# Performance work log

Measured on AMD Instinct MI355X. Metric: run time of the kernel, lower is better.

Reference implementation:

```python
import jax, jax.numpy as jnp
import numpy as np

B, N, M, D = 16, 128, 64, 512
H = 4
K = D // H  # head_dim = 128
L = 3      # num_labels


def setup_inputs() -> dict:
    key = jax.random.key(0)
    ks = jax.random.split(key, 16)
    s = 0.02
    return {
        "word": jax.random.normal(ks[0], (B, N, D), jnp.float32),
        "rel": jax.random.normal(ks[1], (B, M, D), jnp.float32),
        "mask": jnp.ones((B, M), jnp.float32),
        "Wn_w": jax.random.normal(ks[2], (D, D), jnp.float32) * s,
        "Wn_b": jnp.zeros((D,), jnp.float32),
        "Wr_w": jax.random.normal(ks[3], (D, D), jnp.float32) * s,
        "Wr_b": jnp.zeros((D,), jnp.float32),
        "lin_w": jax.random.normal(ks[4], (H, D, K), jnp.float32) * s,
        "lin_b": jnp.zeros((H, K), jnp.float32),
        "score_w": jax.random.normal(ks[5], (H, K), jnp.float32) * s,
        "score_b": jnp.zeros((H,), jnp.float32),
        "final_w": jax.random.normal(ks[6], (D, D), jnp.float32) * s,
        "final_b": jnp.zeros((D,), jnp.float32),
        "fc_w": jax.random.normal(ks[7], (D, L), jnp.float32) * s,
        "fc_b": jnp.zeros((L,), jnp.float32),
    }


def reference(word, rel, mask, Wn_w, Wn_b, Wr_w, Wr_b, lin_w, lin_b,
              score_w, score_b, final_w, final_b, fc_w, fc_b):
    # projections (dropout = identity in eval mode)
    w = word @ Wn_w + Wn_b                     # [B,N,D]
    r = rel @ Wr_w + Wr_b                      # [B,M,D]
    # outer-product hadamard + relu            # [B,N,M,D]
    had = jax.nn.relu(w[:, :, None, :] * r[:, None, :, :])
    # per-head linear projection, vectorized over heads
    t = jnp.einsum('bnmd,hdk->bnmhk', had, lin_w) + lin_b  # [B,N,M,H,K]
    # per-head scalar score + softmax over M (the dim=-1 of [B,N,M])
    s = jnp.einsum('bnmhk,hk->bnmh', t, score_w) + score_b  # [B,N,M,H]
    wts = jax.nn.softmax(s, axis=2) * mask[:, None, :, None]
    # masked weighted sum over M, then mean over N
    head = jnp.einsum('bnmh,bnmhk->bnhk', wts, t)           # [B,N,H,K]
    head = head.mean(axis=1).reshape(head.shape[0], H * K)  # [B,D] (concat heads)
    out = head @ final_w + final_b
    out = jax.nn.relu(out)
    logits = out @ fc_w + fc_b                               # [B,L]
    return logits
```

## Files before the change

kernel.cpp:

```cpp
#include <hip/hip_runtime.h>
#include <math.h>


#define OFF_W   0
#define OFF_R   (2048*512)
#define OFF_V   (OFF_R + 1024*512)
#define OFF_S   (OFF_V + 2048)
#define OFF_G   (OFF_S + 64*8192)
#define OFF_SW  (OFF_G + 64*512)
#define OFF_HM  (OFF_SW + 256)

__global__ __launch_bounds__(256) void proj_gemm(
    const float* __restrict__ word, const float* __restrict__ rel,
    const float* __restrict__ Wn_w, const float* __restrict__ Wn_b,
    const float* __restrict__ Wr_w, const float* __restrict__ Wr_b,
    const float* __restrict__ lin_w, const float* __restrict__ score_w,
    float* __restrict__ ws)
{
    int blk = blockIdx.x;
    if (blk >= 384) {
        int gid = (blk - 384) * 256 + threadIdx.x;
        int h = gid >> 9, d = gid & 511;
        const float* lw = lin_w + (size_t)(h * 512 + d) * 128;
        const float* sw = score_w + h * 128;
        float acc = 0.f;
        #pragma unroll 4
        for (int k = 0; k < 128; k += 4) {
            float4 a = *(const float4*)(lw + k);
            float4 b = *(const float4*)(sw + k);
            acc = fmaf(a.x, b.x, acc); acc = fmaf(a.y, b.y, acc);
            acc = fmaf(a.z, b.z, acc); acc = fmaf(a.w, b.w, acc);
        }
        ws[OFF_V + h * 512 + d] = 0.5f * acc;
        return;
    }
    const float *A, *W, *bias;
    float* C;
    int rowTile, colTile;
    if (blk < 256) {
        A = word; W = Wn_w; bias = Wn_b; C = ws + OFF_W;
        rowTile = blk >> 3; colTile = blk & 7;
    } else {
        int b2 = blk - 256;
        A = rel; W = Wr_w; bias = Wr_b; C = ws + OFF_R;
        rowTile = b2 >> 3; colTile = b2 & 7;
    }
    const int row0 = rowTile * 64, col0 = colTile * 64;

    __shared__ float As[16][68];
    __shared__ float Bs[16][64];

    const int t  = threadIdx.x;
    const int tx = t & 15, ty = t >> 4;
    const int lr = t >> 2, lk = (t & 3) << 2;
    const int bk = t >> 4, bc = (t & 15) << 2;

    float acc[4][4] = {};

    for (int k0 = 0; k0 < 512; k0 += 16) {
        float4 a4 = *(const float4*)(A + (size_t)(row0 + lr) * 512 + k0 + lk);
        As[lk + 0][lr] = a4.x; As[lk + 1][lr] = a4.y;
        As[lk + 2][lr] = a4.z; As[lk + 3][lr] = a4.w;
        *(float4*)&Bs[bk][bc] = *(const float4*)(W + (size_t)(k0 + bk) * 512 + col0 + bc);
        __syncthreads();
        #pragma unroll
        for (int kk = 0; kk < 16; kk++) {
            float4 av = *(float4*)&As[kk][ty << 2];
            float4 bv = *(float4*)&Bs[kk][tx << 2];
            float aa[4] = {av.x, av.y, av.z, av.w};
            float bb[4] = {bv.x, bv.y, bv.z, bv.w};
            #pragma unroll
            for (int i = 0; i < 4; i++)
                #pragma unroll
                for (int j = 0; j < 4; j++)
                    acc[i][j] = fmaf(aa[i], bb[j], acc[i][j]);
        }
        __syncthreads();
    }
    float4 bv = *(const float4*)(bias + col0 + (tx << 2));
    float bb[4] = {bv.x, bv.y, bv.z, bv.w};
    #pragma unroll
    for (int i = 0; i < 4; i++) {
        float4 o;
        o.x = acc[i][0] + bb[0]; o.y = acc[i][1] + bb[1];
        o.z = acc[i][2] + bb[2]; o.w = acc[i][3] + bb[3];
        *(float4*)(C + (size_t)(row0 + (ty << 2) + i) * 512 + col0 + (tx << 2)) = o;
    }
}

__global__ __launch_bounds__(256) void scores_sm(
    const float* __restrict__ mask, float* __restrict__ ws)
{
    const int blk = blockIdx.x;
    const int nq = blk & 3, bh = blk >> 2, h = bh & 3, b = bh >> 2;
    const int n0 = nq * 32;

    const float* wbase = ws + OFF_W + (size_t)(b * 128) * 512;
    const float* rbase = ws + OFF_R + (size_t)(b * 64) * 512;
    float* wtsT = ws + OFF_S + (size_t)bh * 8192;

    __shared__ float v2s[512];
    __shared__ float maskl[64];
    __shared__ float As[16][68], Aa[16][68];
    __shared__ float Bs[16][36], Ba[16][36];
    __shared__ float sl[64][37];
    __shared__ float invl[33];

    const int t = threadIdx.x;
    if (t < 128) *(float4*)&v2s[t * 4] = *(const float4*)(ws + OFF_V + h * 512 + t * 4);
    if (t < 64) maskl[t] = mask[b * 64 + t];
    __syncthreads();

    const int ty = t >> 4, tx = t & 15;
    const int am = t >> 2, akq = (t & 3) * 4;
    const int bn = t >> 2, bkq = (t & 3) * 4;

    float acc[4][2] = {};

    for (int k0 = 0; k0 < 512; k0 += 16) {
        {
            float4 r4 = *(const float4*)(rbase + (size_t)am * 512 + k0 + akq);
            float4 vv = *(const float4*)&v2s[k0 + akq];
            As[akq + 0][am] = r4.x * vv.x; Aa[akq + 0][am] = fabsf(r4.x) * vv.x;
            As[akq + 1][am] = r4.y * vv.y; Aa[akq + 1][am] = fabsf(r4.y) * vv.y;
            As[akq + 2][am] = r4.z * vv.z; Aa[akq + 2][am] = fabsf(r4.z) * vv.z;
            As[akq + 3][am] = r4.w * vv.w; Aa[akq + 3][am] = fabsf(r4.w) * vv.w;
        }
        if (t < 128) {
            float4 w4 = *(const float4*)(wbase + (size_t)(n0 + bn) * 512 + k0 + bkq);
            Bs[bkq + 0][bn] = w4.x; Ba[bkq + 0][bn] = fabsf(w4.x);
            Bs[bkq + 1][bn] = w4.y; Ba[bkq + 1][bn] = fabsf(w4.y);
            Bs[bkq + 2][bn] = w4.z; Ba[bkq + 2][bn] = fabsf(w4.z);
            Bs[bkq + 3][bn] = w4.w; Ba[bkq + 3][bn] = fabsf(w4.w);
        }
        __syncthreads();
        #pragma unroll
        for (int kk = 0; kk < 16; kk++) {
            float4 a  = *(float4*)&As[kk][ty * 4];
            float4 aa = *(float4*)&Aa[kk][ty * 4];
            float2 bv  = *(float2*)&Bs[kk][tx * 2];
            float2 bav = *(float2*)&Ba[kk][tx * 2];
            float a_[4]  = {a.x, a.y, a.z, a.w};
            float aa_[4] = {aa.x, aa.y, aa.z, aa.w};
            #pragma unroll
            for (int i = 0; i < 4; i++) {
                acc[i][0] = fmaf(a_[i], bv.x,  acc[i][0]);
                acc[i][0] = fmaf(aa_[i], bav.x, acc[i][0]);
                acc[i][1] = fmaf(a_[i], bv.y,  acc[i][1]);
                acc[i][1] = fmaf(aa_[i], bav.y, acc[i][1]);
            }
        }
        __syncthreads();
    }
    #pragma unroll
    for (int i = 0; i < 4; i++) {
        sl[ty * 4 + i][tx * 2 + 0] = acc[i][0];
        sl[ty * 4 + i][tx * 2 + 1] = acc[i][1];
    }
    __syncthreads();

    if (t < 32) {
        const int n = t;
        float mx = sl[0][n];
        #pragma unroll
        for (int m = 1; m < 64; m++) mx = fmaxf(mx, sl[m][n]);
        float esum = 0.f, emsum = 0.f;
        #pragma unroll
        for (int m = 0; m < 64; m++) {
            float e = expf(sl[m][n] - mx);
            sl[m][n] = e;
            esum += e;
            emsum = fmaf(e, maskl[m], emsum);
        }
        float inv = 1.0f / esum;
        invl[n] = inv;
        float swq = emsum * inv;
        #pragma unroll
        for (int off = 16; off > 0; off >>= 1)
            swq += __shfl_xor(swq, off);
        if (t == 0) ws[OFF_SW + bh * 4 + nq] = swq;
    }
    __syncthreads();

    const int wn = t >> 3;
    const int wm = (t & 7) * 8;
    const float inv = invl[wn];
    float o[8];
    #pragma unroll
    for (int e2 = 0; e2 < 8; e2++)
        o[e2] = sl[wm + e2][wn] * inv * maskl[wm + e2];
    float4 o0; o0.x = o[0]; o0.y = o[1]; o0.z = o[2]; o0.w = o[3];
    float4 o1; o1.x = o[4]; o1.y = o[5]; o1.z = o[6]; o1.w = o[7];
    *(float4*)(wtsT + (size_t)(n0 + wn) * 64 + wm)     = o0;
    *(float4*)(wtsT + (size_t)(n0 + wn) * 64 + wm + 4) = o1;
}

__global__ __launch_bounds__(256) void gstep_kernel(float* __restrict__ ws)
{
    const int blk = blockIdx.x;
    const int dtile = blk & 7, bh = blk >> 3;
    const int b = bh >> 2;
    const int d0 = dtile * 64;
    const float* wtsT  = ws + OFF_S + (size_t)bh * 8192;
    const float* wbase = ws + OFF_W + (size_t)(b * 128) * 512;
    const float* rbase = ws + OFF_R + (size_t)(b * 64) * 512;

    __shared__ float As[16][68];
    __shared__ float Bs[16][68];
    __shared__ float Ba[16][68];
    __shared__ float red[16][68];

    const int t = threadIdx.x;
    const int tx = t & 15, ty = t >> 4;
    const int an_r = t >> 4, am4 = (t & 15) * 4;
    const int bn = t >> 4, bd4 = (t & 15) * 4;

    float accC[4][4] = {}, accA[4][4] = {};

    for (int n0 = 0; n0 < 128; n0 += 16) {
        *(float4*)&As[an_r][am4] =
            *(const float4*)(wtsT + (size_t)(n0 + an_r) * 64 + am4);
        float4 b4 = *(const float4*)(wbase + (size_t)(n0 + bn) * 512 + d0 + bd4);
        *(float4*)&Bs[bn][bd4] = b4;
        float4 bb; bb.x = fabsf(b4.x); bb.y = fabsf(b4.y);
        bb.z = fabsf(b4.z); bb.w = fabsf(b4.w);
        *(float4*)&Ba[bn][bd4] = bb;
        __syncthreads();
        #pragma unroll
        for (int kk = 0; kk < 16; kk++) {
            float4 av  = *(float4*)&As[kk][ty * 4];
            float4 bv  = *(float4*)&Bs[kk][tx * 4];
            float4 bav = *(float4*)&Ba[kk][tx * 4];
            float av_[4]  = {av.x, av.y, av.z, av.w};
            float bv_[4]  = {bv.x, bv.y, bv.z, bv.w};
            float bav_[4] = {bav.x, bav.y, bav.z, bav.w};
            #pragma unroll
            for (int i = 0; i < 4; i++)
                #pragma unroll
                for (int j = 0; j < 4; j++) {
                    accC[i][j] = fmaf(av_[i], bv_[j],  accC[i][j]);
                    accA[i][j] = fmaf(av_[i], bav_[j], accA[i][j]);
                }
        }
        __syncthreads();
    }
    float g0 = 0.f, g1 = 0.f, g2 = 0.f, g3 = 0.f;
    #pragma unroll
    for (int i = 0; i < 4; i++) {
        float4 rv = *(const float4*)(rbase + (size_t)(ty * 4 + i) * 512 + d0 + tx * 4);
        g0 = fmaf(rv.x, accC[i][0], g0); g0 = fmaf(fabsf(rv.x), accA[i][0], g0);
        g1 = fmaf(rv.y, accC[i][1], g1); g1 = fmaf(fabsf(rv.y), accA[i][1], g1);
        g2 = fmaf(rv.z, accC[i][2], g2); g2 = fmaf(fabsf(rv.z), accA[i][2], g2);
        g3 = fmaf(rv.w, accC[i][3], g3); g3 = fmaf(fabsf(rv.w), accA[i][3], g3);
    }
    float4 gg; gg.x = g0; gg.y = g1; gg.z = g2; gg.w = g3;
    *(float4*)&red[ty][tx * 4] = gg;
    __syncthreads();
    if (t < 64) {
        float s = 0.f;
        #pragma unroll
        for (int q = 0; q < 16; q++) s += red[q][t];
        ws[OFF_G + (size_t)bh * 512 + d0 + t] = 0.5f * s;
    }
}

__global__ __launch_bounds__(256) void headmean_kernel(
    const float* __restrict__ lin_w, const float* __restrict__ lin_b,
    float* __restrict__ ws)
{
    const int blk = blockIdx.x;
    const int kt = blk & 3, bh = blk >> 2, b = bh >> 2, h = bh & 3;
    const int t = threadIdx.x;
    const int dg = t >> 5, kk = t & 31;
    const int k = kt * 32 + kk;

    __shared__ float Gs[512];
    __shared__ float red[8][33];

    Gs[t]       = ws[OFF_G + (size_t)bh * 512 + t];
    Gs[t + 256] = ws[OFF_G + (size_t)bh * 512 + t + 256];
    __syncthreads();

    const float* lwp = lin_w + ((size_t)h * 512 + dg * 64) * 128 + k;
    const float* gp = Gs + dg * 64;
    float acc = 0.f;
    #pragma unroll 8
    for (int d = 0; d < 64; d++)
        acc = fmaf(gp[d], lwp[(size_t)d * 128], acc);
    red[dg][kk] = acc;
    __syncthreads();
    if (t < 32) {
        float s = 0.f;
        #pragma unroll
        for (int q = 0; q < 8; q++) s += red[q][t];
        const float SWv = ws[OFF_SW + bh * 4 + 0] + ws[OFF_SW + bh * 4 + 1]
                        + ws[OFF_SW + bh * 4 + 2] + ws[OFF_SW + bh * 4 + 3];
        s = fmaf(lin_b[h * 128 + kt * 32 + t], SWv, s);
        ws[OFF_HM + (size_t)b * 512 + h * 128 + kt * 32 + t] = s * (1.0f / 128.0f);
    }
}

__global__ __launch_bounds__(256) void final_logits(
    const float* __restrict__ final_w, const float* __restrict__ final_b,
    const float* __restrict__ fc_w, const float* __restrict__ fc_b,
    const float* __restrict__ ws, float* __restrict__ out)
{
    const int blk = blockIdx.x;
    const int jt = blk & 15, b = blk >> 4;
    const int t = threadIdx.x;
    const int dg = t >> 5, jj = t & 31;
    const int j = jt * 32 + jj;

    __shared__ float hs[512];
    __shared__ float red[8][33];
    __shared__ float osl[32];

    hs[t]       = ws[OFF_HM + (size_t)b * 512 + t];
    hs[t + 256] = ws[OFF_HM + (size_t)b * 512 + t + 256];
    __syncthreads();

    const float* fwp = final_w + (size_t)(dg * 64) * 512 + j;
    const float* hp = hs + dg * 64;
    float acc = 0.f;
    #pragma unroll 8
    for (int d = 0; d < 64; d++)
        acc = fmaf(hp[d], fwp[(size_t)d * 512], acc);
    red[dg][jj] = acc;
    __syncthreads();
    if (t < 32) {
        float s = 0.f;
        #pragma unroll
        for (int q = 0; q < 8; q++) s += red[q][t];
        osl[t] = fmaxf(s + final_b[jt * 32 + t], 0.f);
    }
    __syncthreads();
    if (t < 96) {
        const int l = t >> 5, j2 = t & 31;
        float val = osl[j2] * fc_w[(jt * 32 + j2) * 3 + l];
        #pragma unroll
        for (int off = 16; off > 0; off >>= 1)
            val += __shfl_xor(val, off);
        if (j2 == 0) atomicAdd(out + b * 3 + l, val);
    }
    if (jt == 0 && t < 3) atomicAdd(out + b * 3 + t, fc_b[t]);
}

extern "C" void kernel_launch(void* const* d_in, const int* in_sizes, int n_in,
                              void* d_out, int out_size, void* d_ws, size_t ws_size,
                              hipStream_t stream)
{
    const float* word    = (const float*)d_in[0];
    const float* rel     = (const float*)d_in[1];
    const float* mask    = (const float*)d_in[2];
    const float* Wn_w    = (const float*)d_in[3];
    const float* Wn_b    = (const float*)d_in[4];
    const float* Wr_w    = (const float*)d_in[5];
    const float* Wr_b    = (const float*)d_in[6];
    const float* lin_w   = (const float*)d_in[7];
    const float* lin_b   = (const float*)d_in[8];
    const float* score_w = (const float*)d_in[9];
    const float* final_w = (const float*)d_in[11];
    const float* final_b = (const float*)d_in[12];
    const float* fc_w    = (const float*)d_in[13];
    const float* fc_b    = (const float*)d_in[14];
    float* ws  = (float*)d_ws;
    float* out = (float*)d_out;

    hipMemsetAsync(out, 0, 16 * 3 * sizeof(float), stream);

    proj_gemm<<<392, 256, 0, stream>>>(word, rel, Wn_w, Wn_b, Wr_w, Wr_b,
                                       lin_w, score_w, ws);
    scores_sm<<<256, 256, 0, stream>>>(mask, ws);
    gstep_kernel<<<512, 256, 0, stream>>>(ws);
    headmean_kernel<<<256, 256, 0, stream>>>(lin_w, lin_b, ws);
    final_logits<<<256, 256, 0, stream>>>(final_w, final_b, fc_w, fc_b, ws, out);
}
```

Before: 191.2 us.

## Double-buffer score GEMM, parallelize softmax, fuse head-mean and final layers

The score kernel now double-buffers its shared-memory tiles and prefetches the next k-slice into registers, which removes one barrier per iteration. It also recomputes |w| on the fly instead of storing a second tile. The softmax reduction is spread across all 256 threads instead of 32. The head-mean and final/logits kernels are merged into a single 16-block kernel that writes outputs directly, removing the memset, the atomics and one launch. The trade-off is that the fused epilogue runs on only 16 blocks with long serial dot products, so it may underuse the GPU.

Measured after the change: 218.0 us. +14.0%, slower.

```diff
diff --git a/kernel.cpp b/kernel.cpp
--- a/kernel.cpp
+++ b/kernel.cpp
@@ -8,7 +8,6 @@
 #define OFF_S   (OFF_V + 2048)
 #define OFF_G   (OFF_S + 64*8192)
 #define OFF_SW  (OFF_G + 64*512)
-#define OFF_HM  (OFF_SW + 256)
 
 __global__ __launch_bounds__(256) void proj_gemm(
     const float* __restrict__ word, const float* __restrict__ rel,
@@ -101,98 +100,125 @@
 
     __shared__ float v2s[512];
     __shared__ float maskl[64];
-    __shared__ float As[16][68], Aa[16][68];
-    __shared__ float Bs[16][36], Ba[16][36];
-    __shared__ float sl[64][37];
-    __shared__ float invl[33];
+    __shared__ float Arv[2][16][68];
+    __shared__ float Ara[2][16][68];
+    __shared__ float Wl[2][16][36];
+    __shared__ float sl[64][33];
+    __shared__ float pmax[8][33], psum[8][33], pms[8][33];
 
     const int t = threadIdx.x;
     if (t < 128) *(float4*)&v2s[t * 4] = *(const float4*)(ws + OFF_V + h * 512 + t * 4);
     if (t < 64) maskl[t] = mask[b * 64 + t];
-    __syncthreads();
-
-    const int ty = t >> 4, tx = t & 15;
-    const int am = t >> 2, akq = (t & 3) * 4;
-    const int bn = t >> 2, bkq = (t & 3) * 4;
+
+    const int tm = t & 15, tn = t >> 4;
+    const int sm = t >> 2, sk = (t & 3) * 4;
+    const int wn = t >> 2, wk = (t & 3) * 4;
+    __syncthreads();
+
+    {
+        float4 r4 = *(const float4*)(rbase + (size_t)sm * 512 + sk);
+        float4 vv = *(const float4*)&v2s[sk];
+        Arv[0][sk + 0][sm] = r4.x * vv.x; Ara[0][sk + 0][sm] = fabsf(r4.x) * vv.x;
+        Arv[0][sk + 1][sm] = r4.y * vv.y; Ara[0][sk + 1][sm] = fabsf(r4.y) * vv.y;
+        Arv[0][sk + 2][sm] = r4.z * vv.z; Ara[0][sk + 2][sm] = fabsf(r4.z) * vv.z;
+        Arv[0][sk + 3][sm] = r4.w * vv.w; Ara[0][sk + 3][sm] = fabsf(r4.w) * vv.w;
+        if (t < 128) {
+            float4 w4 = *(const float4*)(wbase + (size_t)(n0 + wn) * 512 + wk);
+            Wl[0][wk + 0][wn] = w4.x; Wl[0][wk + 1][wn] = w4.y;
+            Wl[0][wk + 2][wn] = w4.z; Wl[0][wk + 3][wn] = w4.w;
+        }
+    }
+    __syncthreads();
 
     float acc[4][2] = {};
-
-    for (int k0 = 0; k0 < 512; k0 += 16) {
-        {
-            float4 r4 = *(const float4*)(rbase + (size_t)am * 512 + k0 + akq);
-            float4 vv = *(const float4*)&v2s[k0 + akq];
-            As[akq + 0][am] = r4.x * vv.x; Aa[akq + 0][am] = fabsf(r4.x) * vv.x;
-            As[akq + 1][am] = r4.y * vv.y; Aa[akq + 1][am] = fabsf(r4.y) * vv.y;
-            As[akq + 2][am] = r4.z * vv.z; Aa[akq + 2][am] = fabsf(r4.z) * vv.z;
-            As[akq + 3][am] = r4.w * vv.w; Aa[akq + 3][am] = fabsf(r4.w) * vv.w;
-        }
-        if (t < 128) {
-            float4 w4 = *(const float4*)(wbase + (size_t)(n0 + bn) * 512 + k0 + bkq);
-            Bs[bkq + 0][bn] = w4.x; Ba[bkq + 0][bn] = fabsf(w4.x);
-            Bs[bkq + 1][bn] = w4.y; Ba[bkq + 1][bn] = fabsf(w4.y);
-            Bs[bkq + 2][bn] = w4.z; Ba[bkq + 2][bn] = fabsf(w4.z);
-            Bs[bkq + 3][bn] = w4.w; Ba[bkq + 3][bn] = fabsf(w4.w);
-        }
-        __syncthreads();
+    int buf = 0;
+    for (int s = 0; s < 32; s++) {
+        float4 r4n, w4n;
+        const int k0n = (s + 1) * 16;
+        if (s < 31) {
+            r4n = *(const float4*)(rbase + (size_t)sm * 512 + k0n + sk);
+            if (t < 128)
+                w4n = *(const float4*)(wbase + (size_t)(n0 + wn) * 512 + k0n + wk);
+        }
         #pragma unroll
         for (int kk = 0; kk < 16; kk++) {
-            float4 a  = *(float4*)&As[kk][ty * 4];
-            float4 aa = *(float4*)&Aa[kk][ty * 4];
-            float2 bv  = *(float2*)&Bs[kk][tx * 2];
-            float2 bav = *(float2*)&Ba[kk][tx * 2];
-            float a_[4]  = {a.x, a.y, a.z, a.w};
-            float aa_[4] = {aa.x, aa.y, aa.z, aa.w};
-            #pragma unroll
-            for (int i = 0; i < 4; i++) {
-                acc[i][0] = fmaf(a_[i], bv.x,  acc[i][0]);
-                acc[i][0] = fmaf(aa_[i], bav.x, acc[i][0]);
-                acc[i][1] = fmaf(a_[i], bv.y,  acc[i][1]);
-                acc[i][1] = fmaf(aa_[i], bav.y, acc[i][1]);
+            float4 rv = *(float4*)&Arv[buf][kk][tm * 4];
+            float4 ra = *(float4*)&Ara[buf][kk][tm * 4];
+            float2 wv = *(float2*)&Wl[buf][kk][tn * 2];
+            float wax = fabsf(wv.x), way = fabsf(wv.y);
+            acc[0][0] = fmaf(rv.x, wv.x, acc[0][0]); acc[0][0] = fmaf(ra.x, wax, acc[0][0]);
+            acc[1][0] = fmaf(rv.y, wv.x, acc[1][0]); acc[1][0] = fmaf(ra.y, wax, acc[1][0]);
+            acc[2][0] = fmaf(rv.z, wv.x, acc[2][0]); acc[2][0] = fmaf(ra.z, wax, acc[2][0]);
+            acc[3][0] = fmaf(rv.w, wv.x, acc[3][0]); acc[3][0] = fmaf(ra.w, wax, acc[3][0]);
+            acc[0][1] = fmaf(rv.x, wv.y, acc[0][1]); acc[0][1] = fmaf(ra.x, way, acc[0][1]);
+            acc[1][1] = fmaf(rv.y, wv.y, acc[1][1]); acc[1][1] = fmaf(ra.y, way, acc[1][1]);
+            acc[2][1] = fmaf(rv.z, wv.y, acc[2][1]); acc[2][1] = fmaf(ra.z, way, acc[2][1]);
+            acc[3][1] = fmaf(rv.w, wv.y, acc[3][1]); acc[3][1] = fmaf(ra.w, way, acc[3][1]);
+        }
+        if (s < 31) {
+            float4 vv = *(const float4*)&v2s[k0n + sk];
+            const int nb = buf ^ 1;
+            Arv[nb][sk + 0][sm] = r4n.x * vv.x; Ara[nb][sk + 0][sm] = fabsf(r4n.x) * vv.x;
+            Arv[nb][sk + 1][sm] = r4n.y * vv.y; Ara[nb][sk + 1][sm] = fabsf(r4n.y) * vv.y;
+            Arv[nb][sk + 2][sm] = r4n.z * vv.z; Ara[nb][sk + 2][sm] = fabsf(r4n.z) * vv.z;
+            Arv[nb][sk + 3][sm] = r4n.w * vv.w; Ara[nb][sk + 3][sm] = fabsf(r4n.w) * vv.w;
+            if (t < 128) {
+                Wl[nb][wk + 0][wn] = w4n.x; Wl[nb][wk + 1][wn] = w4n.y;
+                Wl[nb][wk + 2][wn] = w4n.z; Wl[nb][wk + 3][wn] = w4n.w;
             }
         }
         __syncthreads();
-    }
+        buf ^= 1;
+    }
+
     #pragma unroll
     for (int i = 0; i < 4; i++) {
-        sl[ty * 4 + i][tx * 2 + 0] = acc[i][0];
-        sl[ty * 4 + i][tx * 2 + 1] = acc[i][1];
-    }
-    __syncthreads();
-
-    if (t < 32) {
-        const int n = t;
-        float mx = sl[0][n];
-        #pragma unroll
-        for (int m = 1; m < 64; m++) mx = fmaxf(mx, sl[m][n]);
-        float esum = 0.f, emsum = 0.f;
-        #pragma unroll
-        for (int m = 0; m < 64; m++) {
-            float e = expf(sl[m][n] - mx);
-            sl[m][n] = e;
-            esum += e;
-            emsum = fmaf(e, maskl[m], emsum);
-        }
-        float inv = 1.0f / esum;
-        invl[n] = inv;
-        float swq = emsum * inv;
-        #pragma unroll
-        for (int off = 16; off > 0; off >>= 1)
-            swq += __shfl_xor(swq, off);
-        if (t == 0) ws[OFF_SW + bh * 4 + nq] = swq;
-    }
-    __syncthreads();
-
-    const int wn = t >> 3;
-    const int wm = (t & 7) * 8;
-    const float inv = invl[wn];
+        sl[tm * 4 + i][tn * 2 + 0] = acc[i][0];
+        sl[tm * 4 + i][tn * 2 + 1] = acc[i][1];
+    }
+    __syncthreads();
+
+    const int col = t & 31, seg = t >> 5;
+    {
+        float mx = sl[seg * 8 + 0][col];
+        #pragma unroll
+        for (int q = 1; q < 8; q++) mx = fmaxf(mx, sl[seg * 8 + q][col]);
+        pmax[seg][col] = mx;
+    }
+    __syncthreads();
+    float gmx = pmax[0][col];
+    #pragma unroll
+    for (int q = 1; q < 8; q++) gmx = fmaxf(gmx, pmax[q][col]);
+    float es[8], ps = 0.f, pm = 0.f;
+    #pragma unroll
+    for (int q = 0; q < 8; q++) {
+        int m = seg * 8 + q;
+        float e = expf(sl[m][col] - gmx);
+        es[q] = e; ps += e; pm = fmaf(e, maskl[m], pm);
+    }
+    psum[seg][col] = ps; pms[seg][col] = pm;
+    __syncthreads();
+    float tot = psum[0][col];
+    #pragma unroll
+    for (int q = 1; q < 8; q++) tot += psum[q][col];
+    const float inv = 1.0f / tot;
     float o[8];
     #pragma unroll
-    for (int e2 = 0; e2 < 8; e2++)
-        o[e2] = sl[wm + e2][wn] * inv * maskl[wm + e2];
+    for (int q = 0; q < 8; q++) o[q] = es[q] * inv * maskl[seg * 8 + q];
     float4 o0; o0.x = o[0]; o0.y = o[1]; o0.z = o[2]; o0.w = o[3];
     float4 o1; o1.x = o[4]; o1.y = o[5]; o1.z = o[6]; o1.w = o[7];
-    *(float4*)(wtsT + (size_t)(n0 + wn) * 64 + wm)     = o0;
-    *(float4*)(wtsT + (size_t)(n0 + wn) * 64 + wm + 4) = o1;
+    *(float4*)(wtsT + (size_t)(n0 + col) * 64 + seg * 8)     = o0;
+    *(float4*)(wtsT + (size_t)(n0 + col) * 64 + seg * 8 + 4) = o1;
+    if (seg == 0) {
+        float pmt = pms[0][col];
+        #pragma unroll
+        for (int q = 1; q < 8; q++) pmt += pms[q][col];
+        float swc = pmt * inv;
+        #pragma unroll
+        for (int off = 16; off > 0; off >>= 1)
+            swc += __shfl_xor(swc, off);
+        if (col == 0) ws[OFF_SW + bh * 4 + nq] = swc;
+    }
 }
 
 __global__ __launch_bounds__(256) void gstep_kernel(float* __restrict__ ws)
@@ -264,85 +290,70 @@
     }
 }
 
-__global__ __launch_bounds__(256) void headmean_kernel(
+__global__ __launch_bounds__(256) void epilogue_kernel(
     const float* __restrict__ lin_w, const float* __restrict__ lin_b,
-    float* __restrict__ ws)
-{
-    const int blk = blockIdx.x;
-    const int kt = blk & 3, bh = blk >> 2, b = bh >> 2, h = bh & 3;
-    const int t = threadIdx.x;
-    const int dg = t >> 5, kk = t & 31;
-    const int k = kt * 32 + kk;
-
-    __shared__ float Gs[512];
-    __shared__ float red[8][33];
-
-    Gs[t]       = ws[OFF_G + (size_t)bh * 512 + t];
-    Gs[t + 256] = ws[OFF_G + (size_t)bh * 512 + t + 256];
-    __syncthreads();
-
-    const float* lwp = lin_w + ((size_t)h * 512 + dg * 64) * 128 + k;
-    const float* gp = Gs + dg * 64;
-    float acc = 0.f;
-    #pragma unroll 8
-    for (int d = 0; d < 64; d++)
-        acc = fmaf(gp[d], lwp[(size_t)d * 128], acc);
-    red[dg][kk] = acc;
-    __syncthreads();
-    if (t < 32) {
-        float s = 0.f;
-        #pragma unroll
-        for (int q = 0; q < 8; q++) s += red[q][t];
-        const float SWv = ws[OFF_SW + bh * 4 + 0] + ws[OFF_SW + bh * 4 + 1]
-                        + ws[OFF_SW + bh * 4 + 2] + ws[OFF_SW + bh * 4 + 3];
-        s = fmaf(lin_b[h * 128 + kt * 32 + t], SWv, s);
-        ws[OFF_HM + (size_t)b * 512 + h * 128 + kt * 32 + t] = s * (1.0f / 128.0f);
-    }
-}
-
-__global__ __launch_bounds__(256) void final_logits(
     const float* __restrict__ final_w, const float* __restrict__ final_b,
     const float* __restrict__ fc_w, const float* __restrict__ fc_b,
     const float* __restrict__ ws, float* __restrict__ out)
 {
-    const int blk = blockIdx.x;
-    const int jt = blk & 15, b = blk >> 4;
-    const int t = threadIdx.x;
-    const int dg = t >> 5, jj = t & 31;
-    const int j = jt * 32 + jj;
-
+    const int b = blockIdx.x, t = threadIdx.x;
+    __shared__ float Gs[2048];
     __shared__ float hs[512];
-    __shared__ float red[8][33];
-    __shared__ float osl[32];
-
-    hs[t]       = ws[OFF_HM + (size_t)b * 512 + t];
-    hs[t + 256] = ws[OFF_HM + (size_t)b * 512 + t + 256];
-    __syncthreads();
-
-    const float* fwp = final_w + (size_t)(dg * 64) * 512 + j;
-    const float* hp = hs + dg * 64;
-    float acc = 0.f;
-    #pragma unroll 8
-    for (int d = 0; d < 64; d++)
-        acc = fmaf(hp[d], fwp[(size_t)d * 512], acc);
-    red[dg][jj] = acc;
-    __syncthreads();
-    if (t < 32) {
-        float s = 0.f;
-        #pragma unroll
-        for (int q = 0; q < 8; q++) s += red[q][t];
-        osl[t] = fmaxf(s + final_b[jt * 32 + t], 0.f);
-    }
-    __syncthreads();
-    if (t < 96) {
-        const int l = t >> 5, j2 = t & 31;
-        float val = osl[j2] * fc_w[(jt * 32 + j2) * 3 + l];
-        #pragma unroll
-        for (int off = 16; off > 0; off >>= 1)
-            val += __shfl_xor(val, off);
-        if (j2 == 0) atomicAdd(out + b * 3 + l, val);
-    }
-    if (jt == 0 && t < 3) atomicAdd(out + b * 3 + t, fc_b[t]);
+    __shared__ float os[512];
+    __shared__ float SWs[4];
+
+    const float* G = ws + OFF_G + (size_t)b * 2048;
+    #pragma unroll
+    for (int i = 0; i < 8; i++) Gs[t + 256 * i] = G[t + 256 * i];
+    if (t < 4) {
+        const float* swq = ws + OFF_SW + (size_t)(b * 4 + t) * 4;
+        SWs[t] = (swq[0] + swq[1]) + (swq[2] + swq[3]);
+    }
+    __syncthreads();
+
+    #pragma unroll
+    for (int i = 0; i < 2; i++) {
+        int idx = t + 256 * i;
+        int h = idx >> 7, k = idx & 127;
+        const float* lwp = lin_w + ((size_t)h * 512) * 128 + k;
+        const float* gp = Gs + h * 512;
+        float a0 = 0.f, a1 = 0.f, a2 = 0.f, a3 = 0.f;
+        for (int d = 0; d < 512; d += 4) {
+            a0 = fmaf(gp[d + 0], lwp[(size_t)(d + 0) * 128], a0);
+            a1 = fmaf(gp[d + 1], lwp[(size_t)(d + 1) * 128], a1);
+            a2 = fmaf(gp[d + 2], lwp[(size_t)(d + 2) * 128], a2);
+            a3 = fmaf(gp[d + 3], lwp[(size_t)(d + 3) * 128], a3);
+        }
+        float acc = (a0 + a1) + (a2 + a3) + lin_b[h * 128 + k] * SWs[h];
+        hs[idx] = acc * (1.0f / 128.0f);
+    }
+    __syncthreads();
+
+    #pragma unroll
+    for (int i = 0; i < 2; i++) {
+        int j = t + 256 * i;
+        const float* fwp = final_w + j;
+        float a0 = 0.f, a1 = 0.f, a2 = 0.f, a3 = 0.f;
+        for (int d = 0; d < 512; d += 4) {
+            a0 = fmaf(hs[d + 0], fwp[(size_t)(d + 0) * 512], a0);
+            a1 = fmaf(hs[d + 1], fwp[(size_t)(d + 1) * 512], a1);
+            a2 = fmaf(hs[d + 2], fwp[(size_t)(d + 2) * 512], a2);
+            a3 = fmaf(hs[d + 3], fwp[(size_t)(d + 3) * 512], a3);
+        }
+        os[j] = fmaxf((a0 + a1) + (a2 + a3) + final_b[j], 0.f);
+    }
+    __syncthreads();
+
+    if (t < 192) {
+        int l = t >> 6, ln = t & 63;
+        float acc = 0.f;
+        for (int i2 = ln; i2 < 512; i2 += 64)
+            acc = fmaf(os[i2], fc_w[i2 * 3 + l], acc);
+        #pragma unroll
+        for (int off = 32; off > 0; off >>= 1)
+            acc += __shfl_xor(acc, off);
+        if (ln == 0) out[b * 3 + l] = acc + fc_b[l];
+    }
 }
 
 extern "C" void kernel_launch(void* const* d_in, const int* in_sizes, int n_in,
@@ -366,12 +377,10 @@
     float* ws  = (float*)d_ws;
     float* out = (float*)d_out;
 
-    hipMemsetAsync(out, 0, 16 * 3 * sizeof(float), stream);
-
     proj_gemm<<<392, 256, 0, stream>>>(word, rel, Wn_w, Wn_b, Wr_w, Wr_b,
                                        lin_w, score_w, ws);
     scores_sm<<<256, 256, 0, stream>>>(mask, ws);
     gstep_kernel<<<512, 256, 0, stream>>>(ws);
-    headmean_kernel<<<256, 256, 0, stream>>>(lin_w, lin_b, ws);
-    final_logits<<<256, 256, 0, stream>>>(final_w, final_b, fc_w, fc_b, ws, out);
-}
+    epilogue_kernel<<<16, 256, 0, stream>>>(lin_w, lin_b, final_w, final_b,
+                                            fc_w, fc_b, ws, out);
+}
```
